# Kernel tuning notes

Hardware: AMD Instinct MI355X
Metric: run time of the kernel (lower is better)

## Reference

```python
import jax, jax.numpy as jnp
import numpy as np

C = 64          # residual channels
N_LAYERS = 30
MAX_STEPS = 200
SQRT2 = 2.0 ** 0.5


def _conv1d(x, W, b, dilation=1, pad=0):
    # x: [B, Cin, T], W: [Cout, Cin, K], b: [Cout]
    y = jax.lax.conv_general_dilated(
        x, W, window_strides=(1,), padding=[(pad, pad)],
        rhs_dilation=(dilation,), dimension_numbers=('NCH', 'OIH', 'NCH'))
    return y + b[None, :, None]


def _silu(x):
    return x * jax.nn.sigmoid(x)


def _emb_table():
    steps = jnp.arange(MAX_STEPS, dtype=jnp.float32)[:, None]      # [200,1]
    dims = jnp.arange(64, dtype=jnp.float32)[None, :]              # [1,64]
    t = steps * 10.0 ** (dims * 4.0 / 63.0)                        # [200,64]
    return jnp.concatenate([jnp.sin(t), jnp.cos(t)], axis=1)       # [200,128]


def setup_inputs() -> dict:
    key = jax.random.key(0)
    ks = jax.random.split(key, 20)
    B, T = 4, 16384
    f32 = jnp.float32
    inp = {
        'audio': jax.random.normal(ks[0], (B, 1, T), dtype=f32),
        'diffusion_step': jax.random.randint(ks[1], (B,), 0, MAX_STEPS),
        # input projection Conv1d(1, 64, 1)
        'in_W': jax.random.normal(ks[2], (C, 1, 1), f32) * 1.0,
        'in_b': jax.random.normal(ks[3], (C,), f32) * 0.01,
        # diffusion embedding MLP 128->512->512
        'p1_W': jax.random.normal(ks[4], (512, 128), f32) * (1.0 / np.sqrt(128)),
        'p1_b': jnp.zeros((512,), f32),
        'p2_W': jax.random.normal(ks[5], (512, 512), f32) * (1.0 / np.sqrt(512)),
        'p2_b': jnp.zeros((512,), f32),
        # per-layer params (stacked over 30 layers)
        'dw_W': jax.random.normal(ks[6], (N_LAYERS, 2 * C, C, 3), f32) * (1.0 / np.sqrt(3 * C)),
        'dw_b': jnp.zeros((N_LAYERS, 2 * C), f32),
        'dp_W': jax.random.normal(ks[7], (N_LAYERS, C, 512), f32) * (1.0 / np.sqrt(512)),
        'dp_b': jnp.zeros((N_LAYERS, C), f32),
        'op_W': jax.random.normal(ks[8], (N_LAYERS, 2 * C, C, 1), f32) * (1.0 / np.sqrt(C)),
        'op_b': jnp.zeros((N_LAYERS, 2 * C), f32),
        # skip projection Conv1d(64,64,1)
        'sk_W': jax.random.normal(ks[9], (C, C, 1), f32) * (1.0 / np.sqrt(C)),
        'sk_b': jnp.zeros((C,), f32),
        # output projection Conv1d(64,1,1), weight zero-init like original
        'out_W': jnp.zeros((1, C, 1), f32),
        'out_b': jax.random.normal(ks[10], (1,), f32) * 0.01,
    }
    return inp


def reference(audio, diffusion_step, in_W, in_b, p1_W, p1_b, p2_W, p2_b,
              dw_W, dw_b, dp_W, dp_b, op_W, op_b, sk_W, sk_b, out_W, out_b):
    x = jax.nn.relu(_conv1d(audio, in_W, in_b))                    # [B,64,T]
    # diffusion embedding
    t = _emb_table()[diffusion_step]                               # [B,128]
    t = _silu(t @ p1_W.T + p1_b)                                   # [B,512]
    t = _silu(t @ p2_W.T + p2_b)                                   # [B,512]
    skip = None
    for i in range(N_LAYERS):
        d = 2 ** (i % 10)
        cond = (t @ dp_W[i].T + dp_b[i])[:, :, None]               # [B,64,1]
        y = _conv1d(x + cond, dw_W[i], dw_b[i], dilation=d, pad=d) # [B,128,T]
        gate, filt = y[:, :C], y[:, C:]
        y = jax.nn.sigmoid(gate) * jnp.tanh(filt)                  # [B,64,T]
        y = _conv1d(y, op_W[i], op_b[i])                           # [B,128,T]
        residual, sk = y[:, :C], y[:, C:]
        x = (x + residual) / SQRT2
        skip = sk if skip is None else skip + sk
    x = skip / np.sqrt(float(N_LAYERS)).astype(np.float32)
    x = jax.nn.relu(_conv1d(x, sk_W, sk_b))
    return _conv1d(x, out_W, out_b)                                # [B,1,T]
```

## Files before the change

kernel.cpp:

```cpp
#include <hip/hip_runtime.h>
#include <math.h>

#define C 64
#define NL 30
#define T 16384
#define B 4

typedef __bf16 bf16_t;
typedef __bf16 bf16x8 __attribute__((ext_vector_type(8)));
typedef __bf16 bf16x4 __attribute__((ext_vector_type(4)));
typedef float f32x4 __attribute__((ext_vector_type(4)));

typedef const __attribute__((address_space(1))) unsigned int glb_u32;
typedef __attribute__((address_space(3))) unsigned int lds_u32;

constexpr float INV_SQRT2   = 0.70710678118654752440f;
constexpr float INV_SQRT_NL = 0.18257418583505537115f;

__device__ __forceinline__ float fsig(float x) {
    return __builtin_amdgcn_rcpf(1.f + __builtin_amdgcn_exp2f(-1.44269504089f * x));
}
__device__ __forceinline__ float ftanh(float x) {
    return fmaf(2.f, __builtin_amdgcn_rcpf(1.f + __builtin_amdgcn_exp2f(-2.88539008178f * x)), -1.f);
}
__device__ __forceinline__ int swz(int off) { return off ^ ((off >> 3) & 0x70); }

__global__ void pack_weights(const float* __restrict__ dw_W,
                             const float* __restrict__ op_W,
                             const float* __restrict__ sk_W,
                             bf16_t* __restrict__ convpk,
                             bf16_t* __restrict__ oppk,
                             bf16_t* __restrict__ skpk) {
    int idx = blockIdx.x * 256 + threadIdx.x;
    const int ndw = NL * 128 * 192;
    const int nop = NL * 128 * 64;
    if (idx < ndw) {
        int k = idx % 192; int r = idx / 192;
        int oc = r % 128;  int l = r / 128;
        int tap = k >> 6, ic = k & 63;
        convpk[idx] = (bf16_t)dw_W[((l * 128 + oc) * 64 + ic) * 3 + tap];
    } else if (idx < ndw + nop) {
        oppk[idx - ndw] = (bf16_t)op_W[idx - ndw];
    } else if (idx < ndw + nop + 4096) {
        int j = idx - ndw - nop;
        skpk[j] = (bf16_t)(sk_W[j] * INV_SQRT_NL);
    }
}

__global__ void cond_embp1(const int* __restrict__ step,
                           const float* __restrict__ p1_W, const float* __restrict__ p1_b,
                           float* __restrict__ h1out) {
    __shared__ float e[128];
    __shared__ float red[256];
    int b = blockIdx.x, blk = blockIdx.y, tid = threadIdx.x;
    int s = step[b];
    if (tid < 128) {
        int d = tid & 63;
        float tf = (float)s * powf(10.f, (float)d * 4.f / 63.f);
        double td = (double)tf;
        e[tid] = (tid < 64) ? (float)sin(td) : (float)cos(td);
    }
    __syncthreads();
    int ol = tid >> 2, q = tid & 3;
    int o = blk * 64 + ol;
    const float4* wr = (const float4*)(p1_W + o * 128 + q * 32);
    const float4* ev = (const float4*)(e + q * 32);
    float a = 0.f;
    #pragma unroll
    for (int j = 0; j < 8; ++j) {
        float4 wv = wr[j]; float4 xv = ev[j];
        a = fmaf(wv.x, xv.x, a); a = fmaf(wv.y, xv.y, a);
        a = fmaf(wv.z, xv.z, a); a = fmaf(wv.w, xv.w, a);
    }
    red[tid] = a;
    __syncthreads();
    if (q == 0) {
        float v = red[tid] + red[tid + 1] + red[tid + 2] + red[tid + 3] + p1_b[o];
        h1out[b * 512 + o] = v / (1.f + expf(-v));
    }
}

__global__ void cond_p2(const float* __restrict__ h1,
                        const float* __restrict__ p2_W, const float* __restrict__ p2_b,
                        float* __restrict__ h2out) {
    __shared__ float red[256];
    int b = blockIdx.x, blk = blockIdx.y, tid = threadIdx.x;
    int ol = tid >> 2, q = tid & 3;
    int o = blk * 64 + ol;
    const float4* wr = (const float4*)(p2_W + o * 512 + q * 128);
    const float4* hv = (const float4*)(h1 + b * 512 + q * 128);
    float a = 0.f;
    #pragma unroll 8
    for (int j = 0; j < 32; ++j) {
        float4 wv = wr[j]; float4 xv = hv[j];
        a = fmaf(wv.x, xv.x, a); a = fmaf(wv.y, xv.y, a);
        a = fmaf(wv.z, xv.z, a); a = fmaf(wv.w, xv.w, a);
    }
    red[tid] = a;
    __syncthreads();
    if (q == 0) {
        float v = red[tid] + red[tid + 1] + red[tid + 2] + red[tid + 3] + p2_b[o];
        h2out[b * 512 + o] = v / (1.f + expf(-v));
    }
}

__global__ void cond_stage2b(const float* __restrict__ h2,
                             const float* __restrict__ dp_W, const float* __restrict__ dp_b,
                             const bf16_t* __restrict__ convpk,
                             const float* __restrict__ dw_b,
                             float* __restrict__ bias2) {
    __shared__ float red[256];
    __shared__ float cond_s[64];
    int l = blockIdx.x, b = blockIdx.y;
    int tid = threadIdx.x;
    {
        int o = tid >> 2, q = tid & 3;
        const float4* wr = (const float4*)(dp_W + ((size_t)l * C + o) * 512 + q * 128);
        const float4* h = (const float4*)(h2 + b * 512 + q * 128);
        float a = 0.f;
        #pragma unroll 8
        for (int j = 0; j < 32; ++j) {
            float4 wv = wr[j]; float4 hv = h[j];
            a = fmaf(wv.x, hv.x, a); a = fmaf(wv.y, hv.y, a);
            a = fmaf(wv.z, hv.z, a); a = fmaf(wv.w, hv.w, a);
        }
        red[tid] = a;
        __syncthreads();
        if (q == 0)
            cond_s[o] = red[tid] + red[tid + 1] + red[tid + 2] + red[tid + 3] + dp_b[l * C + o];
    }
    __syncthreads();
    int oc = tid & 127, kh = tid >> 7;
    const bf16_t* wr = convpk + ((size_t)l * 128 + oc) * 192 + kh * 96;
    float a = kh ? 0.f : dw_b[l * 128 + oc];
    #pragma unroll
    for (int j = 0; j < 96; ++j)
        a = fmaf((float)wr[j], cond_s[(kh * 96 + j) & 63], a);
    __syncthreads();
    red[tid] = a;
    __syncthreads();
    if (tid < 128)
        bias2[(l * B + b) * 128 + tid] = red[tid] + red[tid + 128];
}

__global__ void in_conv(const float* __restrict__ audio,
                        const float* __restrict__ in_W, const float* __restrict__ in_b,
                        bf16_t* __restrict__ x) {
    int idx = blockIdx.x * 256 + threadIdx.x;
    int cb = idx & 7;
    int t = (idx >> 3) & (T - 1);
    int b = idx >> 17;
    float av = audio[b * T + t];
    bf16x8 o;
    #pragma unroll
    for (int j = 0; j < 8; ++j) {
        int c = cb * 8 + j;
        o[j] = (bf16_t)fmaxf(fmaf(in_W[c], av, in_b[c]), 0.f);
    }
    *(bf16x8*)(x + ((size_t)b * T + t) * 64 + cb * 8) = o;
}

__global__ __launch_bounds__(512, 4) void layer_kernel(
    const bf16_t* __restrict__ x_in, bf16_t* __restrict__ x_out, bf16_t* __restrict__ skip,
    const bf16_t* __restrict__ convpk, const bf16_t* __restrict__ oppk,
    const float* __restrict__ bias2, const float* __restrict__ op_b,
    const bf16_t* __restrict__ zpage,
    int layer, int dil, int first)
{
    __shared__ uint4 smem_u[4096];
    char* sm = (char*)smem_u;

    int tid = threadIdx.x;
    int w8 = __builtin_amdgcn_readfirstlane(tid >> 6);
    int wq = w8 & 3;
    int h  = w8 >> 2;
    int l = tid & 63;
    int lr = l & 15;
    int g = l >> 4;
    int b = blockIdx.y;
    int tbase = blockIdx.x * 128;
    const bf16_t* xb = x_in + (size_t)b * T * 64;

    #pragma unroll
    for (int it = 0; it < 6; ++it) {
        int hh = it / 3;
        int slice = it % 3;
        int row = tid >> 3;
        int c16 = l & 7;
        int ts = tbase + hh * 64 + row + (slice - 1) * dil;
        int c16s = c16 ^ (row & 7);
        const bf16_t* src = ((unsigned)ts < (unsigned)T)
            ? (xb + (size_t)ts * 64 + c16s * 8)
            : (zpage + c16s * 8);
        __builtin_amdgcn_global_load_lds(
            (glb_u32*)src,
            (lds_u32*)(sm + it * 8192 + w8 * 1024),
            16, 0, 0);
    }

    bf16x8 cA[2][6];
    const bf16_t* cw = convpk + (size_t)layer * 128 * 192;
    #pragma unroll
    for (int mf = 0; mf < 2; ++mf)
        #pragma unroll
        for (int kf = 0; kf < 6; ++kf)
            cA[mf][kf] = *(const bf16x8*)(cw + (mf * 64 + wq * 16 + lr) * 192 + kf * 32 + g * 8);

    f32x4 acc[2][4];
    const float* b2 = bias2 + (layer * B + b) * 128;
    #pragma unroll
    for (int mf = 0; mf < 2; ++mf) {
        f32x4 bv;
        #pragma unroll
        for (int r = 0; r < 4; ++r) bv[r] = b2[mf * 64 + wq * 16 + g * 4 + r];
        #pragma unroll
        for (int nf = 0; nf < 4; ++nf) acc[mf][nf] = bv;
    }
    __syncthreads();

    int hbase = h * 24576;
    #pragma unroll
    for (int kf = 0; kf < 6; ++kf) {
        int tap = kf >> 1;
        int kc = (kf & 1) * 32;
        bf16x8 Bf[4];
        #pragma unroll
        for (int nf = 0; nf < 4; ++nf) {
            int off = hbase + tap * 8192 + (nf * 16 + lr) * 128 + (kc + g * 8) * 2;
            Bf[nf] = *(const bf16x8*)(sm + swz(off));
        }
        #pragma unroll
        for (int mf = 0; mf < 2; ++mf)
            #pragma unroll
            for (int nf = 0; nf < 4; ++nf)
                acc[mf][nf] = __builtin_amdgcn_mfma_f32_16x16x32_bf16(
                    cA[mf][kf], Bf[nf], acc[mf][nf], 0, 0, 0);
    }

    bf16x8 oA[2][2];
    const bf16_t* ow = oppk + (size_t)layer * 128 * 64;
    #pragma unroll
    for (int mf = 0; mf < 2; ++mf)
        #pragma unroll
        for (int kf = 0; kf < 2; ++kf)
            oA[mf][kf] = *(const bf16x8*)(ow + (mf * 64 + wq * 16 + lr) * 64 + kf * 32 + g * 8);

    int zbase = 49152 + h * 8192;
    #pragma unroll
    for (int nf = 0; nf < 4; ++nf) {
        union { bf16_t hh[4]; uint2 u; } zp;
        #pragma unroll
        for (int r = 0; r < 4; ++r)
            zp.hh[r] = (bf16_t)(fsig(acc[0][nf][r]) * ftanh(acc[1][nf][r]));
        int off = zbase + (nf * 16 + lr) * 128 + (wq * 16 + g * 4) * 2;
        *(uint2*)(sm + swz(off)) = zp.u;
    }
    __syncthreads();

    f32x4 acc2[2][4];
    const float* ob = op_b + layer * 2 * C;
    #pragma unroll
    for (int mf = 0; mf < 2; ++mf) {
        f32x4 bv;
        #pragma unroll
        for (int r = 0; r < 4; ++r) bv[r] = ob[mf * 64 + wq * 16 + g * 4 + r];
        #pragma unroll
        for (int nf = 0; nf < 4; ++nf) acc2[mf][nf] = bv;
    }
    #pragma unroll
    for (int kf = 0; kf < 2; ++kf) {
        bf16x8 Zf[4];
        #pragma unroll
        for (int nf = 0; nf < 4; ++nf) {
            int off = zbase + (nf * 16 + lr) * 128 + (kf * 32 + g * 8) * 2;
            Zf[nf] = *(const bf16x8*)(sm + swz(off));
        }
        #pragma unroll
        for (int mf = 0; mf < 2; ++mf)
            #pragma unroll
            for (int nf = 0; nf < 4; ++nf)
                acc2[mf][nf] = __builtin_amdgcn_mfma_f32_16x16x32_bf16(
                    oA[mf][kf], Zf[nf], acc2[mf][nf], 0, 0, 0);
    }

    size_t bb = (size_t)b * T * 64;
    int t0 = tbase + h * 64;
    #pragma unroll
    for (int nf = 0; nf < 4; ++nf) {
        int t = t0 + nf * 16 + lr;
        int c0 = wq * 16 + g * 4;
        int xoff = hbase + 8192 + (nf * 16 + lr) * 128 + c0 * 2;
        bf16x4 xv = *(const bf16x4*)(sm + swz(xoff));
        bf16x4 ro, so;
        bf16_t* sp = skip + bb + (size_t)t * 64 + c0;
        if (first) {
            #pragma unroll
            for (int r = 0; r < 4; ++r) {
                ro[r] = (bf16_t)(((float)xv[r] + acc2[0][nf][r]) * INV_SQRT2);
                so[r] = (bf16_t)acc2[1][nf][r];
            }
        } else {
            bf16x4 sv = *(const bf16x4*)sp;
            #pragma unroll
            for (int r = 0; r < 4; ++r) {
                ro[r] = (bf16_t)(((float)xv[r] + acc2[0][nf][r]) * INV_SQRT2);
                so[r] = (bf16_t)((float)sv[r] + acc2[1][nf][r]);
            }
        }
        *(bf16x4*)(x_out + bb + (size_t)t * 64 + c0) = ro;
        *(bf16x4*)sp = so;
    }
}

__global__ __launch_bounds__(256) void final_kernel(
    const bf16_t* __restrict__ skip, const bf16_t* __restrict__ skpk,
    const float* __restrict__ sk_b,
    const float* __restrict__ out_W, const float* __restrict__ out_b,
    float* __restrict__ out)
{
    __shared__ uint4 tile_u[512];
    __shared__ float part[16][66];
    unsigned char* sm = (unsigned char*)tile_u;
    int tid = threadIdx.x;
    int w = __builtin_amdgcn_readfirstlane(tid >> 6);
    int l = tid & 63, lr = l & 15, g = l >> 4;
    int b = blockIdx.y, t0 = blockIdx.x * 64;
    const bf16_t* sb = skip + (size_t)b * T * 64;

    #pragma unroll
    for (int it = 0; it < 2; ++it) {
        int q = it * 256 + tid;
        int row = q >> 3, c16 = q & 7;
        uint4 val = *(const uint4*)(sb + (size_t)(t0 + row) * 64 + c16 * 8);
        *(uint4*)(sm + swz(row * 128 + c16 * 16)) = val;
    }

    bf16x8 aS[2];
    #pragma unroll
    for (int kf = 0; kf < 2; ++kf)
        aS[kf] = *(const bf16x8*)(skpk + (w * 16 + lr) * 64 + kf * 32 + g * 8);
    f32x4 acc[4];
    #pragma unroll
    for (int nf = 0; nf < 4; ++nf)
        #pragma unroll
        for (int r = 0; r < 4; ++r) acc[nf][r] = sk_b[w * 16 + g * 4 + r];
    __syncthreads();

    #pragma unroll
    for (int kf = 0; kf < 2; ++kf) {
        bf16x8 Bf[4];
        #pragma unroll
        for (int nf = 0; nf < 4; ++nf) {
            int off = (nf * 16 + lr) * 128 + (kf * 32 + g * 8) * 2;
            Bf[nf] = *(const bf16x8*)(sm + swz(off));
        }
        #pragma unroll
        for (int nf = 0; nf < 4; ++nf)
            acc[nf] = __builtin_amdgcn_mfma_f32_16x16x32_bf16(aS[kf], Bf[nf], acc[nf], 0, 0, 0);
    }

    #pragma unroll
    for (int nf = 0; nf < 4; ++nf) {
        float o = 0.f;
        #pragma unroll
        for (int r = 0; r < 4; ++r)
            o = fmaf(out_W[w * 16 + g * 4 + r], fmaxf(acc[nf][r], 0.f), o);
        part[w * 4 + g][nf * 16 + lr] = o;
    }
    __syncthreads();
    if (tid < 64) {
        float o = out_b[0];
        #pragma unroll
        for (int j = 0; j < 16; ++j) o += part[j][tid];
        out[(size_t)b * T + t0 + tid] = o;
    }
}

extern "C" void kernel_launch(void* const* d_in, const int* in_sizes, int n_in,
                              void* d_out, int out_size, void* d_ws, size_t ws_size,
                              hipStream_t stream) {
    const float* audio = (const float*)d_in[0];
    const int*   dstep = (const int*)d_in[1];
    const float* in_W  = (const float*)d_in[2];
    const float* in_b  = (const float*)d_in[3];
    const float* p1_W  = (const float*)d_in[4];
    const float* p1_b  = (const float*)d_in[5];
    const float* p2_W  = (const float*)d_in[6];
    const float* p2_b  = (const float*)d_in[7];
    const float* dw_W  = (const float*)d_in[8];
    const float* dw_b  = (const float*)d_in[9];
    const float* dp_W  = (const float*)d_in[10];
    const float* dp_b  = (const float*)d_in[11];
    const float* op_W  = (const float*)d_in[12];
    const float* op_b  = (const float*)d_in[13];
    const float* sk_W  = (const float*)d_in[14];
    const float* sk_b  = (const float*)d_in[15];
    const float* out_W = (const float*)d_in[16];
    const float* out_b = (const float*)d_in[17];

    float* ws = (float*)d_ws;
    const size_t NXE = (size_t)B * T * 64;
    float* h1    = ws;
    float* h2    = h1 + B * 512;
    float* bias2 = h2 + B * 512;
    float* zpg   = bias2 + NL * B * 128;
    bf16_t* xA   = (bf16_t*)(zpg + 128);
    bf16_t* xB   = xA + NXE;
    bf16_t* skip = xB + NXE;
    bf16_t* convpk = skip + NXE;
    bf16_t* oppk   = convpk + (size_t)NL * 128 * 192;
    bf16_t* skpk   = oppk + (size_t)NL * 128 * 64;

    hipMemsetAsync(zpg, 0, 512, stream);
    hipLaunchKernelGGL(pack_weights, dim3(3856), dim3(256), 0, stream,
                       dw_W, op_W, sk_W, convpk, oppk, skpk);
    hipLaunchKernelGGL(cond_embp1, dim3(B, 8), dim3(256), 0, stream,
                       dstep, p1_W, p1_b, h1);
    hipLaunchKernelGGL(cond_p2, dim3(B, 8), dim3(256), 0, stream,
                       h1, p2_W, p2_b, h2);
    hipLaunchKernelGGL(cond_stage2b, dim3(NL, B), dim3(256), 0, stream,
                       h2, dp_W, dp_b, convpk, dw_b, bias2);
    hipLaunchKernelGGL(in_conv, dim3(B * T * 8 / 256), dim3(256), 0, stream,
                       audio, in_W, in_b, xA);
    for (int i = 0; i < NL; ++i) {
        bf16_t* xin  = (i & 1) ? xB : xA;
        bf16_t* xout = (i & 1) ? xA : xB;
        int dil = 1 << (i % 10);
        hipLaunchKernelGGL(layer_kernel, dim3(T / 128, B), dim3(512), 0, stream,
                           xin, xout, skip, convpk, oppk, bias2, op_b,
                           (const bf16_t*)zpg, i, dil, (i == 0) ? 1 : 0);
    }
    hipLaunchKernelGGL(final_kernel, dim3(T / 64, B), dim3(256), 0, stream,
                       skip, skpk, sk_b, out_W, out_b, (float*)d_out);
}
```

Baseline: 544.5 us.

## Halve layer block to 4 waves, loop two 64-step subtiles, swizzle tile order

The layer kernel now runs 256 threads (4 waves) per block and handles its 128 time steps as two sequential 64-step subtiles. This halves LDS use per block and loads each conv and output-projection weight fragment once per wave for both subtiles. Block indices are remapped with an XCD-style swizzle so neighbouring tiles go to the same chiplet, and in_conv and final_kernel use the same mapping. The cost is less parallel work per block and an extra barrier between subtiles, with no overlap between the second subtile's loads and the first subtile's compute.

```diff
diff --git a/kernel.cpp b/kernel.cpp
--- a/kernel.cpp
+++ b/kernel.cpp
@@ -143,60 +143,51 @@
         bias2[(l * B + b) * 128 + tid] = red[tid] + red[tid + 128];
 }
 
-__global__ void in_conv(const float* __restrict__ audio,
-                        const float* __restrict__ in_W, const float* __restrict__ in_b,
-                        bf16_t* __restrict__ x) {
-    int idx = blockIdx.x * 256 + threadIdx.x;
-    int cb = idx & 7;
-    int t = (idx >> 3) & (T - 1);
-    int b = idx >> 17;
-    float av = audio[b * T + t];
-    bf16x8 o;
-    #pragma unroll
-    for (int j = 0; j < 8; ++j) {
-        int c = cb * 8 + j;
-        o[j] = (bf16_t)fmaxf(fmaf(in_W[c], av, in_b[c]), 0.f);
-    }
-    *(bf16x8*)(x + ((size_t)b * T + t) * 64 + cb * 8) = o;
-}
-
-__global__ __launch_bounds__(512, 4) void layer_kernel(
+__global__ __launch_bounds__(256) void in_conv(
+    const float* __restrict__ audio,
+    const float* __restrict__ in_W, const float* __restrict__ in_b,
+    bf16_t* __restrict__ x)
+{
+    int bid = blockIdx.x;
+    int tile = ((bid & 7) << 4) + (bid >> 3);
+    int b = blockIdx.y;
+    int t0 = tile * 128;
+    int tid = threadIdx.x;
+    #pragma unroll
+    for (int r = 0; r < 4; ++r) {
+        int q = r * 256 + tid;
+        int row = q >> 3, c16 = q & 7;
+        float av = audio[(size_t)b * T + t0 + row];
+        bf16x8 o;
+        #pragma unroll
+        for (int j = 0; j < 8; ++j) {
+            int c = c16 * 8 + j;
+            o[j] = (bf16_t)fmaxf(fmaf(in_W[c], av, in_b[c]), 0.f);
+        }
+        *(bf16x8*)(x + ((size_t)b * T + t0 + row) * 64 + c16 * 8) = o;
+    }
+}
+
+__global__ __launch_bounds__(256) void layer_kernel(
     const bf16_t* __restrict__ x_in, bf16_t* __restrict__ x_out, bf16_t* __restrict__ skip,
     const bf16_t* __restrict__ convpk, const bf16_t* __restrict__ oppk,
     const float* __restrict__ bias2, const float* __restrict__ op_b,
     const bf16_t* __restrict__ zpage,
     int layer, int dil, int first)
 {
-    __shared__ uint4 smem_u[4096];
+    __shared__ uint4 smem_u[2048];
     char* sm = (char*)smem_u;
 
     int tid = threadIdx.x;
-    int w8 = __builtin_amdgcn_readfirstlane(tid >> 6);
-    int wq = w8 & 3;
-    int h  = w8 >> 2;
+    int w = __builtin_amdgcn_readfirstlane(tid >> 6);
     int l = tid & 63;
     int lr = l & 15;
     int g = l >> 4;
     int b = blockIdx.y;
-    int tbase = blockIdx.x * 128;
+    int bid = blockIdx.x;
+    int tile = ((bid & 7) << 4) + (bid >> 3);
+    int tbase = tile * 128;
     const bf16_t* xb = x_in + (size_t)b * T * 64;
-
-    #pragma unroll
-    for (int it = 0; it < 6; ++it) {
-        int hh = it / 3;
-        int slice = it % 3;
-        int row = tid >> 3;
-        int c16 = l & 7;
-        int ts = tbase + hh * 64 + row + (slice - 1) * dil;
-        int c16s = c16 ^ (row & 7);
-        const bf16_t* src = ((unsigned)ts < (unsigned)T)
-            ? (xb + (size_t)ts * 64 + c16s * 8)
-            : (zpage + c16s * 8);
-        __builtin_amdgcn_global_load_lds(
-            (glb_u32*)src,
-            (lds_u32*)(sm + it * 8192 + w8 * 1024),
-            16, 0, 0);
-    }
 
     bf16x8 cA[2][6];
     const bf16_t* cw = convpk + (size_t)layer * 128 * 192;
@@ -204,111 +195,125 @@
     for (int mf = 0; mf < 2; ++mf)
         #pragma unroll
         for (int kf = 0; kf < 6; ++kf)
-            cA[mf][kf] = *(const bf16x8*)(cw + (mf * 64 + wq * 16 + lr) * 192 + kf * 32 + g * 8);
-
-    f32x4 acc[2][4];
-    const float* b2 = bias2 + (layer * B + b) * 128;
-    #pragma unroll
-    for (int mf = 0; mf < 2; ++mf) {
-        f32x4 bv;
-        #pragma unroll
-        for (int r = 0; r < 4; ++r) bv[r] = b2[mf * 64 + wq * 16 + g * 4 + r];
-        #pragma unroll
-        for (int nf = 0; nf < 4; ++nf) acc[mf][nf] = bv;
-    }
-    __syncthreads();
-
-    int hbase = h * 24576;
-    #pragma unroll
-    for (int kf = 0; kf < 6; ++kf) {
-        int tap = kf >> 1;
-        int kc = (kf & 1) * 32;
-        bf16x8 Bf[4];
-        #pragma unroll
-        for (int nf = 0; nf < 4; ++nf) {
-            int off = hbase + tap * 8192 + (nf * 16 + lr) * 128 + (kc + g * 8) * 2;
-            Bf[nf] = *(const bf16x8*)(sm + swz(off));
-        }
-        #pragma unroll
-        for (int mf = 0; mf < 2; ++mf)
-            #pragma unroll
-            for (int nf = 0; nf < 4; ++nf)
-                acc[mf][nf] = __builtin_amdgcn_mfma_f32_16x16x32_bf16(
-                    cA[mf][kf], Bf[nf], acc[mf][nf], 0, 0, 0);
-    }
-
+            cA[mf][kf] = *(const bf16x8*)(cw + (mf * 64 + w * 16 + lr) * 192 + kf * 32 + g * 8);
     bf16x8 oA[2][2];
     const bf16_t* ow = oppk + (size_t)layer * 128 * 64;
     #pragma unroll
     for (int mf = 0; mf < 2; ++mf)
         #pragma unroll
         for (int kf = 0; kf < 2; ++kf)
-            oA[mf][kf] = *(const bf16x8*)(ow + (mf * 64 + wq * 16 + lr) * 64 + kf * 32 + g * 8);
-
-    int zbase = 49152 + h * 8192;
-    #pragma unroll
-    for (int nf = 0; nf < 4; ++nf) {
-        union { bf16_t hh[4]; uint2 u; } zp;
-        #pragma unroll
-        for (int r = 0; r < 4; ++r)
-            zp.hh[r] = (bf16_t)(fsig(acc[0][nf][r]) * ftanh(acc[1][nf][r]));
-        int off = zbase + (nf * 16 + lr) * 128 + (wq * 16 + g * 4) * 2;
-        *(uint2*)(sm + swz(off)) = zp.u;
-    }
-    __syncthreads();
-
-    f32x4 acc2[2][4];
+            oA[mf][kf] = *(const bf16x8*)(ow + (mf * 64 + w * 16 + lr) * 64 + kf * 32 + g * 8);
+    f32x4 bC[2], bO[2];
+    const float* b2 = bias2 + (layer * B + b) * 128;
     const float* ob = op_b + layer * 2 * C;
     #pragma unroll
-    for (int mf = 0; mf < 2; ++mf) {
-        f32x4 bv;
-        #pragma unroll
-        for (int r = 0; r < 4; ++r) bv[r] = ob[mf * 64 + wq * 16 + g * 4 + r];
-        #pragma unroll
-        for (int nf = 0; nf < 4; ++nf) acc2[mf][nf] = bv;
-    }
-    #pragma unroll
-    for (int kf = 0; kf < 2; ++kf) {
-        bf16x8 Zf[4];
+    for (int mf = 0; mf < 2; ++mf)
+        #pragma unroll
+        for (int r = 0; r < 4; ++r) {
+            bC[mf][r] = b2[mf * 64 + w * 16 + g * 4 + r];
+            bO[mf][r] = ob[mf * 64 + w * 16 + g * 4 + r];
+        }
+
+    size_t bb = (size_t)b * T * 64;
+
+    for (int st = 0; st < 2; ++st) {
+        int t0 = tbase + st * 64;
+
+        #pragma unroll
+        for (int it = 0; it < 6; ++it) {
+            int qq = it * 256 + tid;
+            int slice = qq >> 9, row = (qq >> 3) & 63, c16 = qq & 7;
+            int ts = t0 + row + (slice - 1) * dil;
+            int c16s = c16 ^ (row & 7);
+            const bf16_t* src = ((unsigned)ts < (unsigned)T)
+                ? (xb + (size_t)ts * 64 + c16s * 8)
+                : (zpage + c16s * 8);
+            __builtin_amdgcn_global_load_lds((glb_u32*)src,
+                (lds_u32*)(sm + it * 4096 + w * 1024), 16, 0, 0);
+        }
+        __syncthreads();
+
+        f32x4 acc[2][4];
+        #pragma unroll
+        for (int mf = 0; mf < 2; ++mf)
+            #pragma unroll
+            for (int nf = 0; nf < 4; ++nf) acc[mf][nf] = bC[mf];
+        #pragma unroll
+        for (int kf = 0; kf < 6; ++kf) {
+            int tap = kf >> 1;
+            int kc = (kf & 1) * 32;
+            bf16x8 Bf[4];
+            #pragma unroll
+            for (int nf = 0; nf < 4; ++nf) {
+                int off = tap * 8192 + (nf * 16 + lr) * 128 + (kc + g * 8) * 2;
+                Bf[nf] = *(const bf16x8*)(sm + swz(off));
+            }
+            #pragma unroll
+            for (int mf = 0; mf < 2; ++mf)
+                #pragma unroll
+                for (int nf = 0; nf < 4; ++nf)
+                    acc[mf][nf] = __builtin_amdgcn_mfma_f32_16x16x32_bf16(
+                        cA[mf][kf], Bf[nf], acc[mf][nf], 0, 0, 0);
+        }
+
         #pragma unroll
         for (int nf = 0; nf < 4; ++nf) {
-            int off = zbase + (nf * 16 + lr) * 128 + (kf * 32 + g * 8) * 2;
-            Zf[nf] = *(const bf16x8*)(sm + swz(off));
-        }
+            union { bf16_t hh[4]; uint2 u; } zp;
+            #pragma unroll
+            for (int r = 0; r < 4; ++r)
+                zp.hh[r] = (bf16_t)(fsig(acc[0][nf][r]) * ftanh(acc[1][nf][r]));
+            int off = 24576 + (nf * 16 + lr) * 128 + (w * 16 + g * 4) * 2;
+            *(uint2*)(sm + swz(off)) = zp.u;
+        }
+        __syncthreads();
+
+        f32x4 acc2[2][4];
         #pragma unroll
         for (int mf = 0; mf < 2; ++mf)
             #pragma unroll
-            for (int nf = 0; nf < 4; ++nf)
-                acc2[mf][nf] = __builtin_amdgcn_mfma_f32_16x16x32_bf16(
-                    oA[mf][kf], Zf[nf], acc2[mf][nf], 0, 0, 0);
-    }
-
-    size_t bb = (size_t)b * T * 64;
-    int t0 = tbase + h * 64;
-    #pragma unroll
-    for (int nf = 0; nf < 4; ++nf) {
-        int t = t0 + nf * 16 + lr;
-        int c0 = wq * 16 + g * 4;
-        int xoff = hbase + 8192 + (nf * 16 + lr) * 128 + c0 * 2;
-        bf16x4 xv = *(const bf16x4*)(sm + swz(xoff));
-        bf16x4 ro, so;
-        bf16_t* sp = skip + bb + (size_t)t * 64 + c0;
-        if (first) {
-            #pragma unroll
-            for (int r = 0; r < 4; ++r) {
-                ro[r] = (bf16_t)(((float)xv[r] + acc2[0][nf][r]) * INV_SQRT2);
-                so[r] = (bf16_t)acc2[1][nf][r];
+            for (int nf = 0; nf < 4; ++nf) acc2[mf][nf] = bO[mf];
+        #pragma unroll
+        for (int kf = 0; kf < 2; ++kf) {
+            bf16x8 Zf[4];
+            #pragma unroll
+            for (int nf = 0; nf < 4; ++nf) {
+                int off = 24576 + (nf * 16 + lr) * 128 + (kf * 32 + g * 8) * 2;
+                Zf[nf] = *(const bf16x8*)(sm + swz(off));
             }
-        } else {
-            bf16x4 sv = *(const bf16x4*)sp;
-            #pragma unroll
-            for (int r = 0; r < 4; ++r) {
-                ro[r] = (bf16_t)(((float)xv[r] + acc2[0][nf][r]) * INV_SQRT2);
-                so[r] = (bf16_t)((float)sv[r] + acc2[1][nf][r]);
+            #pragma unroll
+            for (int mf = 0; mf < 2; ++mf)
+                #pragma unroll
+                for (int nf = 0; nf < 4; ++nf)
+                    acc2[mf][nf] = __builtin_amdgcn_mfma_f32_16x16x32_bf16(
+                        oA[mf][kf], Zf[nf], acc2[mf][nf], 0, 0, 0);
+        }
+
+        #pragma unroll
+        for (int nf = 0; nf < 4; ++nf) {
+            int t = t0 + nf * 16 + lr;
+            int c0 = w * 16 + g * 4;
+            int xoff = 8192 + (nf * 16 + lr) * 128 + c0 * 2;
+            bf16x4 xv = *(const bf16x4*)(sm + swz(xoff));
+            bf16x4 ro, so;
+            bf16_t* sp = skip + bb + (size_t)t * 64 + c0;
+            if (first) {
+                #pragma unroll
+                for (int r = 0; r < 4; ++r) {
+                    ro[r] = (bf16_t)(((float)xv[r] + acc2[0][nf][r]) * INV_SQRT2);
+                    so[r] = (bf16_t)acc2[1][nf][r];
+                }
+            } else {
+                bf16x4 sv = *(const bf16x4*)sp;
+                #pragma unroll
+                for (int r = 0; r < 4; ++r) {
+                    ro[r] = (bf16_t)(((float)xv[r] + acc2[0][nf][r]) * INV_SQRT2);
+                    so[r] = (bf16_t)((float)sv[r] + acc2[1][nf][r]);
+                }
             }
-        }
-        *(bf16x4*)(x_out + bb + (size_t)t * 64 + c0) = ro;
-        *(bf16x4*)sp = so;
+            *(bf16x4*)(x_out + bb + (size_t)t * 64 + c0) = ro;
+            *(bf16x4*)sp = so;
+        }
+        if (st == 0) __syncthreads();
     }
 }
 
@@ -324,7 +329,9 @@
     int tid = threadIdx.x;
     int w = __builtin_amdgcn_readfirstlane(tid >> 6);
     int l = tid & 63, lr = l & 15, g = l >> 4;
-    int b = blockIdx.y, t0 = blockIdx.x * 64;
+    int bid = blockIdx.x;
+    int tile = ((bid & 7) << 5) + (bid >> 3);
+    int b = blockIdx.y, t0 = tile * 64;
     const bf16_t* sb = skip + (size_t)b * T * 64;
 
     #pragma unroll
@@ -420,16 +427,19 @@
                        h1, p2_W, p2_b, h2);
     hipLaunchKernelGGL(cond_stage2b, dim3(NL, B), dim3(256), 0, stream,
                        h2, dp_W, dp_b, convpk, dw_b, bias2);
-    hipLaunchKernelGGL(in_conv, dim3(B * T * 8 / 256), dim3(256), 0, stream,
+    hipLaunchKernelGGL(in_conv, dim3(128, B), dim3(256), 0, stream,
                        audio, in_W, in_b, xA);
+
+    bf16_t* bufs[2] = { xA, xB };
+    int cur = 0;
+    const bf16_t* zpgc = (const bf16_t*)zpg;
     for (int i = 0; i < NL; ++i) {
-        bf16_t* xin  = (i & 1) ? xB : xA;
-        bf16_t* xout = (i & 1) ? xA : xB;
         int dil = 1 << (i % 10);
-        hipLaunchKernelGGL(layer_kernel, dim3(T / 128, B), dim3(512), 0, stream,
-                           xin, xout, skip, convpk, oppk, bias2, op_b,
-                           (const bf16_t*)zpg, i, dil, (i == 0) ? 1 : 0);
-    }
-    hipLaunchKernelGGL(final_kernel, dim3(T / 64, B), dim3(256), 0, stream,
+        hipLaunchKernelGGL(layer_kernel, dim3(128, B), dim3(256), 0, stream,
+                           bufs[cur], bufs[cur ^ 1], skip, convpk, oppk,
+                           bias2, op_b, zpgc, i, dil, (i == 0) ? 1 : 0);
+        cur ^= 1;
+    }
+    hipLaunchKernelGGL(final_kernel, dim3(256, B), dim3(256), 0, stream,
                        skip, skpk, sk_b, out_W, out_b, (float*)d_out);
 }
```

Result: faster. 475.9 us (-12.6%).
